# Performance work log

Hardware: AMD Instinct MI355X
Metric: run time of the kernel (lower is better)

The kernel has to match this reference:

```python
import jax, jax.numpy as jnp
import numpy as np

N = 50000      # nodes
E = 800000     # edges (avg degree 16)
IN, H, OUT = 128, 128, 64
NEG_SLOPE = 0.01  # F.leaky_relu default


def _glorot(key, shape):
    lim = float(np.sqrt(6.0 / (shape[0] + shape[1])))
    return jax.random.uniform(key, shape, jnp.float32, -lim, lim)


def setup_inputs() -> dict:
    key = jax.random.key(0)
    ks = jax.random.split(key, 12)
    x = jax.random.normal(ks[0], (N, IN), jnp.float32)
    edge_index = jax.random.randint(ks[1], (2, E), 0, N, dtype=jnp.int64)
    edge_weight = jax.random.uniform(ks[2], (E,), jnp.float32)
    params = {}
    dims = [(IN, H), (H, H), (H, H), (H, OUT)]
    for i, (di, do) in enumerate(dims, start=1):
        params[f"W{i}"] = _glorot(ks[2 + i], (di, do))
        params[f"b{i}"] = jnp.zeros((do,), jnp.float32)
    return {"x": x, "edge_index": edge_index, "edge_weight": edge_weight, **params}


def _gcn_norm(edge_index, edge_weight, n):
    # PyG gcn_norm: add self-loops with weight 1, symmetric D^-1/2 A D^-1/2
    loop = jnp.arange(n, dtype=edge_index.dtype)
    row = jnp.concatenate([edge_index[0], loop])   # source
    col = jnp.concatenate([edge_index[1], loop])   # target
    w = jnp.concatenate([edge_weight, jnp.ones((n,), edge_weight.dtype)])
    deg = jax.ops.segment_sum(w, col, num_segments=n)
    dinv = jnp.where(deg > 0, jax.lax.rsqrt(deg), 0.0)
    norm = dinv[row] * w * dinv[col]
    return row, col, norm


def _gcn_conv(x, W, b, row, col, norm, n):
    h = x @ W                                   # [N, out] dense GEMM
    msg = h[row] * norm[:, None]                # gather + edge scale  [E+N, out]
    out = jax.ops.segment_sum(msg, col, num_segments=n)  # scatter-add
    return out + b


def reference(x, edge_index, edge_weight, W1, b1, W2, b2, W3, b3, W4, b4):
    n = x.shape[0]
    row, col, norm = _gcn_norm(edge_index, edge_weight, n)  # identical for all layers
    h = _gcn_conv(x, W1, b1, row, col, norm, n)
    h = jax.nn.leaky_relu(h, NEG_SLOPE)
    # dropout (p=0.25) is identity in eval mode
    h = _gcn_conv(h, W2, b2, row, col, norm, n)
    h = jax.nn.leaky_relu(h, NEG_SLOPE)
    h = _gcn_conv(h, W3, b3, row, col, norm, n)
    h = jax.nn.leaky_relu(h, NEG_SLOPE)
    h = _gcn_conv(h, W4, b4, row, col, norm, n)
    return h
```

## Files before the change

### kernel.cpp

```cpp
#include <hip/hip_runtime.h>
#include <hip/hip_bf16.h>


#define CAP 64


template <int OUTD>
__device__ __forceinline__ void gemm_body(const float* __restrict__ A,
                                          const float* __restrict__ W,
                                          float* __restrict__ C, int nrows, int bid) {
    constexpr int CW = OUTD / 16;
    constexpr int WF4 = (32 * OUTD / 4) / 256;
    __shared__ float As[32][132];
    __shared__ float Ws[32][OUTD];
    const int t = threadIdx.x;
    const int rowbase = bid * 128;
    const int tx = t & 15, ty = t >> 4;
    const int r0 = ty * 8, c0 = tx * CW;

    float acc[8][CW];
    #pragma unroll
    for (int i = 0; i < 8; ++i)
        #pragma unroll
        for (int j = 0; j < CW; ++j) acc[i][j] = 0.f;

    const int arow = t >> 3, akq = t & 7;

    auto loadA = [&](int kt, int row) -> float4 {
        int gr = rowbase + row;
        if (gr < nrows) return *(const float4*)&A[(size_t)gr * 128 + kt * 32 + akq * 4];
        return make_float4(0.f, 0.f, 0.f, 0.f);
    };
    auto stA = [&](int row, float4 v) {
        As[akq * 4 + 0][row] = v.x;
        As[akq * 4 + 1][row] = v.y;
        As[akq * 4 + 2][row] = v.z;
        As[akq * 4 + 3][row] = v.w;
    };

    #pragma unroll
    for (int u = 0; u < 4; ++u) stA(arow + u * 32, loadA(0, arow + u * 32));
    #pragma unroll
    for (int u = 0; u < WF4; ++u) {
        int idx = t + u * 256;
        int k = idx / (OUTD / 4), cq = idx % (OUTD / 4);
        *(float4*)&Ws[k][cq * 4] = *(const float4*)&W[(size_t)k * OUTD + cq * 4];
    }
    __syncthreads();

    float4 pa[4], pw[WF4];
    #pragma unroll
    for (int kt = 0; kt < 4; ++kt) {
        if (kt < 3) {
            #pragma unroll
            for (int u = 0; u < 4; ++u) pa[u] = loadA(kt + 1, arow + u * 32);
            #pragma unroll
            for (int u = 0; u < WF4; ++u) {
                int idx = t + u * 256;
                int k = idx / (OUTD / 4), cq = idx % (OUTD / 4);
                pw[u] = *(const float4*)&W[(size_t)((kt + 1) * 32 + k) * OUTD + cq * 4];
            }
        }
        #pragma unroll 8
        for (int k = 0; k < 32; ++k) {
            float4 a0 = *(const float4*)&As[k][r0];
            float4 a1 = *(const float4*)&As[k][r0 + 4];
            float w[CW];
            #pragma unroll
            for (int j = 0; j < CW; j += 4)
                *(float4*)&w[j] = *(const float4*)&Ws[k][c0 + j];
            float ar[8] = {a0.x, a0.y, a0.z, a0.w, a1.x, a1.y, a1.z, a1.w};
            #pragma unroll
            for (int i = 0; i < 8; ++i)
                #pragma unroll
                for (int j = 0; j < CW; ++j)
                    acc[i][j] += ar[i] * w[j];
        }
        __syncthreads();
        if (kt < 3) {
            #pragma unroll
            for (int u = 0; u < 4; ++u) stA(arow + u * 32, pa[u]);
            #pragma unroll
            for (int u = 0; u < WF4; ++u) {
                int idx = t + u * 256;
                int k = idx / (OUTD / 4), cq = idx % (OUTD / 4);
                *(float4*)&Ws[k][cq * 4] = pw[u];
            }
            __syncthreads();
        }
    }

    #pragma unroll
    for (int i = 0; i < 8; ++i) {
        int gr = rowbase + r0 + i;
        if (gr < nrows) {
            #pragma unroll
            for (int j = 0; j < CW; j += 4)
                *(float4*)&C[(size_t)gr * OUTD + c0 + j] = *(float4*)&acc[i][j];
        }
    }
}

template <int OUTD>
__global__ __launch_bounds__(256, 3) void gemm_k(const float* __restrict__ A,
                                                 const float* __restrict__ W,
                                                 float* __restrict__ C, int nrows) {
    gemm_body<OUTD>(A, W, C, nrows, blockIdx.x);
}

__global__ __launch_bounds__(256, 3) void gemm1_fill_k(
        const float* __restrict__ A, const float* __restrict__ W,
        float* __restrict__ C, int nrows, int gb,
        const int* __restrict__ ei, const float* __restrict__ ew,
        int* __restrict__ fillc, int2* __restrict__ ed, int E) {
    if ((int)blockIdx.x < gb) {
        gemm_body<128>(A, W, C, nrows, blockIdx.x);
        return;
    }
    int e = (blockIdx.x - gb) * 256 + threadIdx.x;
    if (e >= E) return;
    int r = ei[e];
    int c = ei[E + e];
    int pos = atomicAdd(&fillc[c], 1);
    if (pos < CAP) {
        ed[(size_t)c * CAP + pos] = make_int2(r, __float_as_int(ew[e]));
    }
}

__global__ void fillcap_k(const int* __restrict__ ei, const float* __restrict__ ew,
                          int* __restrict__ fillc, int2* __restrict__ ed, int E) {
    int e = blockIdx.x * 256 + threadIdx.x;
    if (e >= E) return;
    int r = ei[e];
    int c = ei[E + e];
    int pos = atomicAdd(&fillc[c], 1);
    if (pos < CAP) {
        ed[(size_t)c * CAP + pos] = make_int2(r, __float_as_int(ew[e]));
    }
}

__global__ void segdeg_k(const int* __restrict__ fillc, const int2* __restrict__ ed,
                         float* __restrict__ dinv, int n) {
    int t = blockIdx.x * 256 + threadIdx.x;
    int node = t >> 4, l = t & 15;
    if (node >= n) return;
    int len = min(fillc[node], CAP);
    float s = 0.f;
    for (int i = l; i < len; i += 16) s += __int_as_float(ed[(size_t)node * CAP + i].y);
    #pragma unroll
    for (int d = 1; d < 16; d <<= 1) s += __shfl_xor(s, d);
    if (l == 0) dinv[node] = rsqrtf(s + 1.0f);
}

__global__ void nrmfix_k(const int* __restrict__ fillc, int2* __restrict__ ed,
                         const float* __restrict__ dinv, int n) {
    int t = blockIdx.x * 256 + threadIdx.x;
    int node = t >> 4, l = t & 15;
    if (node >= n) return;
    int len = min(fillc[node], CAP);
    float dc = dinv[node];
    for (int i = l; i < len; i += 16) {
        size_t idx = (size_t)node * CAP + i;
        int2 d = ed[idx];
        ((float*)&ed[idx])[1] = dinv[d.x] * __int_as_float(d.y) * dc;
    }
}


template <bool LEAKY>
__global__ __launch_bounds__(256) void aggcap128_k(
        const float* __restrict__ h, const int* __restrict__ fillc,
        const int2* __restrict__ ed, const float* __restrict__ dinv,
        const float* __restrict__ bias, float* __restrict__ out, int n) {
    int node = blockIdx.x * 4 + (threadIdx.x >> 6);
    if (node >= n) return;
    int lane = threadIdx.x & 63;
    int half = lane >> 5;
    int q = lane & 31;
    size_t beg = (size_t)node * CAP;
    int len = min(fillc[node], CAP);
    float4 acc = make_float4(0.f, 0.f, 0.f, 0.f);
    int e = 0;
    for (; e + 16 <= len; e += 16) {
        int2 d[8];
        #pragma unroll
        for (int u = 0; u < 8; ++u) d[u] = ed[beg + e + 2 * u + half];
        float4 v[8];
        #pragma unroll
        for (int u = 0; u < 8; ++u)
            v[u] = *(const float4*)&h[(size_t)d[u].x * 128 + q * 4];
        #pragma unroll
        for (int u = 0; u < 8; ++u) {
            float w = __int_as_float(d[u].y);
            acc.x += w * v[u].x; acc.y += w * v[u].y;
            acc.z += w * v[u].z; acc.w += w * v[u].w;
        }
    }
    for (; e + 8 <= len; e += 8) {
        int2 d0 = ed[beg + e + 0 + half];
        int2 d1 = ed[beg + e + 2 + half];
        int2 d2 = ed[beg + e + 4 + half];
        int2 d3 = ed[beg + e + 6 + half];
        float4 v0 = *(const float4*)&h[(size_t)d0.x * 128 + q * 4];
        float4 v1 = *(const float4*)&h[(size_t)d1.x * 128 + q * 4];
        float4 v2 = *(const float4*)&h[(size_t)d2.x * 128 + q * 4];
        float4 v3 = *(const float4*)&h[(size_t)d3.x * 128 + q * 4];
        float w0 = __int_as_float(d0.y), w1 = __int_as_float(d1.y);
        float w2 = __int_as_float(d2.y), w3 = __int_as_float(d3.y);
        acc.x += w0*v0.x; acc.y += w0*v0.y; acc.z += w0*v0.z; acc.w += w0*v0.w;
        acc.x += w1*v1.x; acc.y += w1*v1.y; acc.z += w1*v1.z; acc.w += w1*v1.w;
        acc.x += w2*v2.x; acc.y += w2*v2.y; acc.z += w2*v2.z; acc.w += w2*v2.w;
        acc.x += w3*v3.x; acc.y += w3*v3.y; acc.z += w3*v3.z; acc.w += w3*v3.w;
    }
    if (e < len) {
        #pragma unroll
        for (int t = 0; t < 4; ++t) {
            int j = e + 2 * t + half;
            bool ok = j < len;
            int2 d = ed[beg + (ok ? j : 0)];
            float w = ok ? __int_as_float(d.y) : 0.f;
            int sr = ok ? d.x : node;
            float4 v = *(const float4*)&h[(size_t)sr * 128 + q * 4];
            acc.x += w*v.x; acc.y += w*v.y; acc.z += w*v.z; acc.w += w*v.w;
        }
    }
    acc.x += __shfl_xor(acc.x, 32);
    acc.y += __shfl_xor(acc.y, 32);
    acc.z += __shfl_xor(acc.z, 32);
    acc.w += __shfl_xor(acc.w, 32);
    float di = dinv[node];
    float ws = di * di;
    float4 hv = *(const float4*)&h[(size_t)node * 128 + q * 4];
    float4 bb = *(const float4*)&bias[q * 4];
    acc.x += ws*hv.x + bb.x;
    acc.y += ws*hv.y + bb.y;
    acc.z += ws*hv.z + bb.z;
    acc.w += ws*hv.w + bb.w;
    if (LEAKY) {
        acc.x = acc.x > 0.f ? acc.x : 0.01f * acc.x;
        acc.y = acc.y > 0.f ? acc.y : 0.01f * acc.y;
        acc.z = acc.z > 0.f ? acc.z : 0.01f * acc.z;
        acc.w = acc.w > 0.f ? acc.w : 0.01f * acc.w;
    }
    if (half == 0) *(float4*)&out[(size_t)node * 128 + q * 4] = acc;
}

__global__ __launch_bounds__(256) void aggcap64_k(
        const float* __restrict__ h, const int* __restrict__ fillc,
        const int2* __restrict__ ed, const float* __restrict__ dinv,
        const float* __restrict__ bias, float* __restrict__ out, int n) {
    int node = blockIdx.x * 4 + (threadIdx.x >> 6);
    if (node >= n) return;
    int lane = threadIdx.x & 63;
    int qtr = lane >> 4;
    int q = lane & 15;
    size_t beg = (size_t)node * CAP;
    int len = min(fillc[node], CAP);
    float4 acc = make_float4(0.f, 0.f, 0.f, 0.f);
    int e = 0;
    for (; e + 16 <= len; e += 16) {
        int2 d[4];
        #pragma unroll
        for (int u = 0; u < 4; ++u) d[u] = ed[beg + e + 4 * u + qtr];
        float4 v[4];
        #pragma unroll
        for (int u = 0; u < 4; ++u)
            v[u] = *(const float4*)&h[(size_t)d[u].x * 64 + q * 4];
        #pragma unroll
        for (int u = 0; u < 4; ++u) {
            float w = __int_as_float(d[u].y);
            acc.x += w * v[u].x; acc.y += w * v[u].y;
            acc.z += w * v[u].z; acc.w += w * v[u].w;
        }
    }
    for (; e + 8 <= len; e += 8) {
        int2 d0 = ed[beg + e + 0 + qtr];
        int2 d1 = ed[beg + e + 4 + qtr];
        float4 v0 = *(const float4*)&h[(size_t)d0.x * 64 + q * 4];
        float4 v1 = *(const float4*)&h[(size_t)d1.x * 64 + q * 4];
        float w0 = __int_as_float(d0.y), w1 = __int_as_float(d1.y);
        acc.x += w0*v0.x; acc.y += w0*v0.y; acc.z += w0*v0.z; acc.w += w0*v0.w;
        acc.x += w1*v1.x; acc.y += w1*v1.y; acc.z += w1*v1.z; acc.w += w1*v1.w;
    }
    if (e < len) {
        #pragma unroll
        for (int t = 0; t < 2; ++t) {
            int j = e + 4 * t + qtr;
            bool ok = j < len;
            int2 d = ed[beg + (ok ? j : 0)];
            float w = ok ? __int_as_float(d.y) : 0.f;
            int sr = ok ? d.x : node;
            float4 v = *(const float4*)&h[(size_t)sr * 64 + q * 4];
            acc.x += w*v.x; acc.y += w*v.y; acc.z += w*v.z; acc.w += w*v.w;
        }
    }
    acc.x += __shfl_xor(acc.x, 16);
    acc.y += __shfl_xor(acc.y, 16);
    acc.z += __shfl_xor(acc.z, 16);
    acc.w += __shfl_xor(acc.w, 16);
    acc.x += __shfl_xor(acc.x, 32);
    acc.y += __shfl_xor(acc.y, 32);
    acc.z += __shfl_xor(acc.z, 32);
    acc.w += __shfl_xor(acc.w, 32);
    float di = dinv[node];
    float ws = di * di;
    float4 hv = *(const float4*)&h[(size_t)node * 64 + q * 4];
    float4 bb = *(const float4*)&bias[q * 4];
    acc.x += ws*hv.x + bb.x;
    acc.y += ws*hv.y + bb.y;
    acc.z += ws*hv.z + bb.z;
    acc.w += ws*hv.w + bb.w;
    if (qtr == 0) *(float4*)&out[(size_t)node * 64 + q * 4] = acc;
}


__global__ void deg_cnt_k(const int* __restrict__ ei, const float* __restrict__ ew,
                          float* __restrict__ deg, int* __restrict__ cnt, int E) {
    int e = blockIdx.x * 256 + threadIdx.x;
    if (e >= E) return;
    int c = ei[E + e];
    atomicAdd(&deg[c], ew[e]);
    atomicAdd(&cnt[c], 1);
}

__global__ void dinv_k(float* __restrict__ d, int n) {
    int i = blockIdx.x * 256 + threadIdx.x;
    if (i >= n) return;
    d[i] = rsqrtf(d[i] + 1.0f);
}

__global__ void scan_blocks_k(const int* __restrict__ cnt, int* __restrict__ rowptr,
                              int* __restrict__ partials, int n) {
    int gid = blockIdx.x * 1024 + threadIdx.x;
    int v = (gid < n) ? cnt[gid] : 0;
    int lane = threadIdx.x & 63, wid = threadIdx.x >> 6;
    int x = v;
    #pragma unroll
    for (int d = 1; d < 64; d <<= 1) {
        int y = __shfl_up(x, d);
        if (lane >= d) x += y;
    }
    __shared__ int wsum[16];
    if (lane == 63) wsum[wid] = x;
    __syncthreads();
    if (wid == 0 && lane < 16) {
        int s = wsum[lane];
        #pragma unroll
        for (int d = 1; d < 16; d <<= 1) {
            int y = __shfl_up(s, d);
            if (lane >= d) s += y;
        }
        wsum[lane] = s;
    }
    __syncthreads();
    int inc = x + (wid > 0 ? wsum[wid - 1] : 0);
    if (gid < n) rowptr[gid] = inc - v;
    if (threadIdx.x == 1023) partials[blockIdx.x] = inc;
}

__global__ void scan_part_k(int* __restrict__ p, int nb) {
    int lane = threadIdx.x;
    int v = (lane < nb) ? p[lane] : 0;
    int x = v;
    #pragma unroll
    for (int d = 1; d < 64; d <<= 1) {
        int y = __shfl_up(x, d);
        if (lane >= d) x += y;
    }
    if (lane < nb) p[lane] = x - v;
    if (lane == 63) p[nb] = x;
}

__global__ void scan_add_k(int* __restrict__ rowptr, const int* __restrict__ p,
                           int n, int nb) {
    int i = blockIdx.x * 1024 + threadIdx.x;
    if (i < n) rowptr[i] += p[blockIdx.x];
    if (i == 0) rowptr[n] = p[nb];
}

__global__ void fill_k(const int* __restrict__ ei, const float* __restrict__ ew,
                       const float* __restrict__ dinv, const int* __restrict__ rowptr,
                       int* __restrict__ fillc, int* __restrict__ src,
                       float* __restrict__ nrm, int E) {
    int e = blockIdx.x * 256 + threadIdx.x;
    if (e >= E) return;
    int r = ei[e];
    int c = ei[E + e];
    int pos = rowptr[c] + atomicAdd(&fillc[c], 1);
    src[pos] = r;
    nrm[pos] = dinv[r] * ew[e] * dinv[c];
}

template <bool LEAKY>
__global__ __launch_bounds__(256) void agg128_k(
        const float* __restrict__ h, const int* __restrict__ rowptr,
        const int* __restrict__ src, const float* __restrict__ nrm,
        const float* __restrict__ dinv, const float* __restrict__ bias,
        float* __restrict__ out, int n) {
    int node = blockIdx.x * 4 + (threadIdx.x >> 6);
    if (node >= n) return;
    int lane = threadIdx.x & 63;
    int beg = rowptr[node], end = rowptr[node + 1];
    float2 acc = make_float2(0.f, 0.f);
    int e = beg;
    for (; e + 4 <= end; e += 4) {
        int s0 = src[e], s1 = src[e + 1], s2 = src[e + 2], s3 = src[e + 3];
        float w0 = nrm[e], w1 = nrm[e + 1], w2 = nrm[e + 2], w3 = nrm[e + 3];
        float2 v0 = *(const float2*)&h[(size_t)s0 * 128 + lane * 2];
        float2 v1 = *(const float2*)&h[(size_t)s1 * 128 + lane * 2];
        float2 v2 = *(const float2*)&h[(size_t)s2 * 128 + lane * 2];
        float2 v3 = *(const float2*)&h[(size_t)s3 * 128 + lane * 2];
        acc.x += w0 * v0.x; acc.y += w0 * v0.y;
        acc.x += w1 * v1.x; acc.y += w1 * v1.y;
        acc.x += w2 * v2.x; acc.y += w2 * v2.y;
        acc.x += w3 * v3.x; acc.y += w3 * v3.y;
    }
    for (; e < end; ++e) {
        int s = src[e];
        float w = nrm[e];
        float2 hv = *(const float2*)&h[(size_t)s * 128 + lane * 2];
        acc.x += w * hv.x;
        acc.y += w * hv.y;
    }
    float di = dinv[node];
    float ws = di * di;
    float2 hv = *(const float2*)&h[(size_t)node * 128 + lane * 2];
    acc.x += ws * hv.x;
    acc.y += ws * hv.y;
    float2 bb = *(const float2*)&bias[lane * 2];
    acc.x += bb.x;
    acc.y += bb.y;
    if (LEAKY) {
        acc.x = acc.x > 0.f ? acc.x : 0.01f * acc.x;
        acc.y = acc.y > 0.f ? acc.y : 0.01f * acc.y;
    }
    *(float2*)&out[(size_t)node * 128 + lane * 2] = acc;
}

__global__ __launch_bounds__(256) void agg64_k(
        const float* __restrict__ h, const int* __restrict__ rowptr,
        const int* __restrict__ src, const float* __restrict__ nrm,
        const float* __restrict__ dinv, const float* __restrict__ bias,
        float* __restrict__ out, int n) {
    int node = blockIdx.x * 4 + (threadIdx.x >> 6);
    if (node >= n) return;
    int lane = threadIdx.x & 63;
    int beg = rowptr[node], end = rowptr[node + 1];
    float acc = 0.f;
    int e = beg;
    for (; e + 4 <= end; e += 4) {
        int s0 = src[e], s1 = src[e + 1], s2 = src[e + 2], s3 = src[e + 3];
        float w0 = nrm[e], w1 = nrm[e + 1], w2 = nrm[e + 2], w3 = nrm[e + 3];
        acc += w0 * h[(size_t)s0 * 64 + lane];
        acc += w1 * h[(size_t)s1 * 64 + lane];
        acc += w2 * h[(size_t)s2 * 64 + lane];
        acc += w3 * h[(size_t)s3 * 64 + lane];
    }
    for (; e < end; ++e) {
        acc += nrm[e] * h[(size_t)src[e] * 64 + lane];
    }
    float di = dinv[node];
    acc += di * di * h[(size_t)node * 64 + lane];
    acc += bias[lane];
    out[(size_t)node * 64 + lane] = acc;
}


extern "C" void kernel_launch(void* const* d_in, const int* in_sizes, int n_in,
                              void* d_out, int out_size, void* d_ws, size_t ws_size,
                              hipStream_t stream) {
    const float* x  = (const float*)d_in[0];
    const int* ei   = (const int*)d_in[1];
    const float* ew = (const float*)d_in[2];
    const float* W1 = (const float*)d_in[3];
    const float* b1 = (const float*)d_in[4];
    const float* W2 = (const float*)d_in[5];
    const float* b2 = (const float*)d_in[6];
    const float* W3 = (const float*)d_in[7];
    const float* b3 = (const float*)d_in[8];
    const float* W4 = (const float*)d_in[9];
    const float* b4 = (const float*)d_in[10];

    const int N = in_sizes[0] / 128;
    const int E = in_sizes[1] / 2;

    auto alignup = [](size_t o) { return (o + 255) & ~(size_t)255; };
    char* ws = (char*)d_ws;
    (void)n_in; (void)out_size;

    int eb = (E + 255) / 256;
    int gb = (N + 127) / 128;
    int ab = (N + 3) / 4;
    int qb = (N * 16 + 255) / 256;

    size_t off = 0;
    float* dinv  = (float*)(ws + off); off = alignup(off + (size_t)N * 4);
    int*   fillc = (int*)(ws + off);   off = alignup(off + (size_t)N * 4);
    size_t zb_cap = off;
    int2*  ed    = (int2*)(ws + off);  off = alignup(off + (size_t)N * CAP * 8);
    float* hbufC = (float*)(ws + off); off = alignup(off + (size_t)N * 128 * 4);
    float* featC = (float*)(ws + off); off = alignup(off + (size_t)N * 128 * 4);
    size_t need_cap = off;

    if (need_cap <= ws_size) {
        hipMemsetAsync(d_ws, 0, zb_cap, stream);
        gemm1_fill_k<<<gb + eb, 256, 0, stream>>>(x, W1, hbufC, N, gb,
                                                  ei, ew, fillc, ed, E);
        segdeg_k<<<qb, 256, 0, stream>>>(fillc, ed, dinv, N);
        nrmfix_k<<<qb, 256, 0, stream>>>(fillc, ed, dinv, N);

        aggcap128_k<true><<<ab, 256, 0, stream>>>(hbufC, fillc, ed, dinv, b1, featC, N);
        gemm_k<128><<<gb, 256, 0, stream>>>(featC, W2, hbufC, N);
        aggcap128_k<true><<<ab, 256, 0, stream>>>(hbufC, fillc, ed, dinv, b2, featC, N);
        gemm_k<128><<<gb, 256, 0, stream>>>(featC, W3, hbufC, N);
        aggcap128_k<true><<<ab, 256, 0, stream>>>(hbufC, fillc, ed, dinv, b3, featC, N);
        gemm_k<64><<<gb, 256, 0, stream>>>(featC, W4, hbufC, N);
        aggcap64_k<<<ab, 256, 0, stream>>>(hbufC, fillc, ed, dinv, b4, (float*)d_out, N);
        return;
    }

    off = 0;
    float* deg   = (float*)(ws + off); off = alignup(off + (size_t)N * 4);
    int*   cnt   = (int*)(ws + off);   off = alignup(off + (size_t)N * 4);
    int*   fillc2= (int*)(ws + off);   off = alignup(off + (size_t)N * 4);
    size_t zbytes = off;
    int*   rowptr = (int*)(ws + off);  off = alignup(off + (size_t)(N + 1) * 4);
    int*   parts  = (int*)(ws + off);  off = alignup(off + 64 * 4);
    int*   srcA   = (int*)(ws + off);  off = alignup(off + (size_t)E * 4);
    float* nrm    = (float*)(ws + off); off = alignup(off + (size_t)E * 4);
    float* hbuf   = (float*)(ws + off); off = alignup(off + (size_t)N * 128 * 4);
    float* feat   = (float*)(ws + off); off = alignup(off + (size_t)N * 128 * 4);

    hipMemsetAsync(d_ws, 0, zbytes, stream);

    int nb = (N + 255) / 256;
    int sb = (N + 1023) / 1024;

    deg_cnt_k<<<eb, 256, 0, stream>>>(ei, ew, deg, cnt, E);
    dinv_k<<<nb, 256, 0, stream>>>(deg, N);
    scan_blocks_k<<<sb, 1024, 0, stream>>>(cnt, rowptr, parts, N);
    scan_part_k<<<1, 64, 0, stream>>>(parts, sb);
    scan_add_k<<<sb, 1024, 0, stream>>>(rowptr, parts, N, sb);
    fill_k<<<eb, 256, 0, stream>>>(ei, ew, deg, rowptr, fillc2, srcA, nrm, E);

    gemm_k<128><<<gb, 256, 0, stream>>>(x, W1, hbuf, N);
    agg128_k<true><<<ab, 256, 0, stream>>>(hbuf, rowptr, srcA, nrm, deg, b1, feat, N);
    gemm_k<128><<<gb, 256, 0, stream>>>(feat, W2, hbuf, N);
    agg128_k<true><<<ab, 256, 0, stream>>>(hbuf, rowptr, srcA, nrm, deg, b2, feat, N);
    gemm_k<128><<<gb, 256, 0, stream>>>(feat, W3, hbuf, N);
    agg128_k<true><<<ab, 256, 0, stream>>>(hbuf, rowptr, srcA, nrm, deg, b3, feat, N);
    gemm_k<64><<<gb, 256, 0, stream>>>(feat, W4, hbuf, N);
    agg64_k<<<ab, 256, 0, stream>>>(hbuf, rowptr, srcA, nrm, deg, b4, (float*)d_out, N);
}
```

Measured before the change: 360.7 us.

## Shrink GEMM tile to 64 rows and drop 16-wide aggregation unroll

The GEMM tile goes from 128 to 64 rows per block, with a 4x4 (or 4x8) micro-tile per thread, and launch bounds rise to 4 waves per SIMD. This gives more blocks and higher occupancy but less register reuse per thread. The aggregation kernels lose their 16-edge unrolled loop and now use the 8-edge loop, which keeps fewer gathers in flight. The unused fillcap_k kernel is also removed.

```diff
diff --git a/kernel.cpp b/kernel.cpp
--- a/kernel.cpp
+++ b/kernel.cpp
@@ -9,20 +9,20 @@
 __device__ __forceinline__ void gemm_body(const float* __restrict__ A,
                                           const float* __restrict__ W,
                                           float* __restrict__ C, int nrows, int bid) {
-    constexpr int CW = OUTD / 16;
+    constexpr int NB = OUTD / 64;
     constexpr int WF4 = (32 * OUTD / 4) / 256;
-    __shared__ float As[32][132];
+    __shared__ float As[32][68];
     __shared__ float Ws[32][OUTD];
     const int t = threadIdx.x;
-    const int rowbase = bid * 128;
+    const int rowbase = bid * 64;
     const int tx = t & 15, ty = t >> 4;
-    const int r0 = ty * 8, c0 = tx * CW;
-
-    float acc[8][CW];
-    #pragma unroll
-    for (int i = 0; i < 8; ++i)
+    const int r0 = ty * 4, c0 = tx * 4;
+
+    float acc[4][4 * NB];
+    #pragma unroll
+    for (int i = 0; i < 4; ++i)
         #pragma unroll
-        for (int j = 0; j < CW; ++j) acc[i][j] = 0.f;
+        for (int j = 0; j < 4 * NB; ++j) acc[i][j] = 0.f;
 
     const int arow = t >> 3, akq = t & 7;
 
@@ -38,8 +38,8 @@
         As[akq * 4 + 3][row] = v.w;
     };
 
-    #pragma unroll
-    for (int u = 0; u < 4; ++u) stA(arow + u * 32, loadA(0, arow + u * 32));
+    stA(arow, loadA(0, arow));
+    stA(arow + 32, loadA(0, arow + 32));
     #pragma unroll
     for (int u = 0; u < WF4; ++u) {
         int idx = t + u * 256;
@@ -48,12 +48,12 @@
     }
     __syncthreads();
 
-    float4 pa[4], pw[WF4];
+    float4 pa0, pa1, pw[WF4];
     #pragma unroll
     for (int kt = 0; kt < 4; ++kt) {
         if (kt < 3) {
-            #pragma unroll
-            for (int u = 0; u < 4; ++u) pa[u] = loadA(kt + 1, arow + u * 32);
+            pa0 = loadA(kt + 1, arow);
+            pa1 = loadA(kt + 1, arow + 32);
             #pragma unroll
             for (int u = 0; u < WF4; ++u) {
                 int idx = t + u * 256;
@@ -63,23 +63,29 @@
         }
         #pragma unroll 8
         for (int k = 0; k < 32; ++k) {
-            float4 a0 = *(const float4*)&As[k][r0];
-            float4 a1 = *(const float4*)&As[k][r0 + 4];
-            float w[CW];
+            float4 a = *(const float4*)&As[k][r0];
+            float4 w0 = *(const float4*)&Ws[k][c0];
+            float ar[4] = {a.x, a.y, a.z, a.w};
+            float wr[4] = {w0.x, w0.y, w0.z, w0.w};
             #pragma unroll
-            for (int j = 0; j < CW; j += 4)
-                *(float4*)&w[j] = *(const float4*)&Ws[k][c0 + j];
-            float ar[8] = {a0.x, a0.y, a0.z, a0.w, a1.x, a1.y, a1.z, a1.w};
-            #pragma unroll
-            for (int i = 0; i < 8; ++i)
+            for (int i = 0; i < 4; ++i)
                 #pragma unroll
-                for (int j = 0; j < CW; ++j)
-                    acc[i][j] += ar[i] * w[j];
+                for (int j = 0; j < 4; ++j)
+                    acc[i][j] += ar[i] * wr[j];
+            if constexpr (NB == 2) {
+                float4 w1 = *(const float4*)&Ws[k][64 + c0];
+                float w1r[4] = {w1.x, w1.y, w1.z, w1.w};
+                #pragma unroll
+                for (int i = 0; i < 4; ++i)
+                    #pragma unroll
+                    for (int j = 0; j < 4; ++j)
+                        acc[i][4 + j] += ar[i] * w1r[j];
+            }
         }
         __syncthreads();
         if (kt < 3) {
-            #pragma unroll
-            for (int u = 0; u < 4; ++u) stA(arow + u * 32, pa[u]);
+            stA(arow, pa0);
+            stA(arow + 32, pa1);
             #pragma unroll
             for (int u = 0; u < WF4; ++u) {
                 int idx = t + u * 256;
@@ -91,24 +97,24 @@
     }
 
     #pragma unroll
-    for (int i = 0; i < 8; ++i) {
+    for (int i = 0; i < 4; ++i) {
         int gr = rowbase + r0 + i;
         if (gr < nrows) {
-            #pragma unroll
-            for (int j = 0; j < CW; j += 4)
-                *(float4*)&C[(size_t)gr * OUTD + c0 + j] = *(float4*)&acc[i][j];
+            *(float4*)&C[(size_t)gr * OUTD + c0] = *(float4*)&acc[i][0];
+            if constexpr (NB == 2)
+                *(float4*)&C[(size_t)gr * OUTD + 64 + c0] = *(float4*)&acc[i][4];
         }
     }
 }
 
 template <int OUTD>
-__global__ __launch_bounds__(256, 3) void gemm_k(const float* __restrict__ A,
+__global__ __launch_bounds__(256, 4) void gemm_k(const float* __restrict__ A,
                                                  const float* __restrict__ W,
                                                  float* __restrict__ C, int nrows) {
     gemm_body<OUTD>(A, W, C, nrows, blockIdx.x);
 }
 
-__global__ __launch_bounds__(256, 3) void gemm1_fill_k(
+__global__ __launch_bounds__(256, 4) void gemm1_fill_k(
         const float* __restrict__ A, const float* __restrict__ W,
         float* __restrict__ C, int nrows, int gb,
         const int* __restrict__ ei, const float* __restrict__ ew,
@@ -118,18 +124,6 @@
         return;
     }
     int e = (blockIdx.x - gb) * 256 + threadIdx.x;
-    if (e >= E) return;
-    int r = ei[e];
-    int c = ei[E + e];
-    int pos = atomicAdd(&fillc[c], 1);
-    if (pos < CAP) {
-        ed[(size_t)c * CAP + pos] = make_int2(r, __float_as_int(ew[e]));
-    }
-}
-
-__global__ void fillcap_k(const int* __restrict__ ei, const float* __restrict__ ew,
-                          int* __restrict__ fillc, int2* __restrict__ ed, int E) {
-    int e = blockIdx.x * 256 + threadIdx.x;
     if (e >= E) return;
     int r = ei[e];
     int c = ei[E + e];
@@ -181,21 +175,6 @@
     int len = min(fillc[node], CAP);
     float4 acc = make_float4(0.f, 0.f, 0.f, 0.f);
     int e = 0;
-    for (; e + 16 <= len; e += 16) {
-        int2 d[8];
-        #pragma unroll
-        for (int u = 0; u < 8; ++u) d[u] = ed[beg + e + 2 * u + half];
-        float4 v[8];
-        #pragma unroll
-        for (int u = 0; u < 8; ++u)
-            v[u] = *(const float4*)&h[(size_t)d[u].x * 128 + q * 4];
-        #pragma unroll
-        for (int u = 0; u < 8; ++u) {
-            float w = __int_as_float(d[u].y);
-            acc.x += w * v[u].x; acc.y += w * v[u].y;
-            acc.z += w * v[u].z; acc.w += w * v[u].w;
-        }
-    }
     for (; e + 8 <= len; e += 8) {
         int2 d0 = ed[beg + e + 0 + half];
         int2 d1 = ed[beg + e + 2 + half];
@@ -258,21 +237,6 @@
     int len = min(fillc[node], CAP);
     float4 acc = make_float4(0.f, 0.f, 0.f, 0.f);
     int e = 0;
-    for (; e + 16 <= len; e += 16) {
-        int2 d[4];
-        #pragma unroll
-        for (int u = 0; u < 4; ++u) d[u] = ed[beg + e + 4 * u + qtr];
-        float4 v[4];
-        #pragma unroll
-        for (int u = 0; u < 4; ++u)
-            v[u] = *(const float4*)&h[(size_t)d[u].x * 64 + q * 4];
-        #pragma unroll
-        for (int u = 0; u < 4; ++u) {
-            float w = __int_as_float(d[u].y);
-            acc.x += w * v[u].x; acc.y += w * v[u].y;
-            acc.z += w * v[u].z; acc.w += w * v[u].w;
-        }
-    }
     for (; e + 8 <= len; e += 8) {
         int2 d0 = ed[beg + e + 0 + qtr];
         int2 d1 = ed[beg + e + 4 + qtr];
@@ -489,7 +453,7 @@
     (void)n_in; (void)out_size;
 
     int eb = (E + 255) / 256;
-    int gb = (N + 127) / 128;
+    int gb = (N + 63) / 64;
     int ab = (N + 3) / 4;
     int qb = (N * 16 + 255) / 256;
 
```

Measured after the change: 360.4 us. No clear change (-0.1%).
